# Kernel optimization log

Measured on AMD Instinct MI355X. Metric: run time of the kernel, lower is better.

The kernel has to match this reference:

```python
import jax, jax.numpy as jnp
import numpy as np

B, T = 512, 100
STATE, LATENT, HIDDEN, EMBED, ACT = 200, 30, 200, 1024, 6


def _lin(k, out_dim, in_dim):
    return jax.random.normal(k, (out_dim, in_dim), jnp.float32) / np.sqrt(in_dim)


def setup_inputs() -> dict:
    key = jax.random.key(0)
    ks = jax.random.split(key, 12)
    return {
        "e": jax.random.normal(ks[0], (B, T + 1, EMBED), jnp.float32),
        "u": jax.random.normal(ks[1], (B, T, ACT), jnp.float32),
        "lat_act_W": _lin(ks[2], STATE, LATENT + ACT),
        "lat_act_b": jnp.zeros((STATE,), jnp.float32),
        "gru_Wih": _lin(ks[3], 3 * STATE, STATE),
        "gru_Whh": _lin(ks[4], 3 * STATE, STATE),
        "gru_bih": jnp.zeros((3 * STATE,), jnp.float32),
        "gru_bhh": jnp.zeros((3 * STATE,), jnp.float32),
        "prior1_W": _lin(ks[5], HIDDEN, STATE),
        "prior1_b": jnp.zeros((HIDDEN,), jnp.float32),
        "prior_m_W": _lin(ks[6], LATENT, HIDDEN),
        "prior_m_b": jnp.zeros((LATENT,), jnp.float32),
        "prior_s_W": _lin(ks[7], LATENT, HIDDEN),
        "prior_s_b": jnp.zeros((LATENT,), jnp.float32),
        "post1_W": _lin(ks[8], HIDDEN, STATE + EMBED),
        "post1_b": jnp.zeros((HIDDEN,), jnp.float32),
        "post_m_W": _lin(ks[9], LATENT, HIDDEN),
        "post_m_b": jnp.zeros((LATENT,), jnp.float32),
        "post_s_W": _lin(ks[10], LATENT, HIDDEN),
        "post_s_b": jnp.zeros((LATENT,), jnp.float32),
    }


def _std(raw):
    # softplus(raw) + 0.1, clamped to [1e-6, 10.0]
    return jnp.clip(jax.nn.softplus(raw) + 0.1, 1e-6, 10.0)


def reference(e, u, lat_act_W, lat_act_b, gru_Wih, gru_Whh, gru_bih, gru_bhh,
              prior1_W, prior1_b, prior_m_W, prior_m_b, prior_s_W, prior_s_b,
              post1_W, post1_b, post_m_W, post_m_b, post_s_W, post_s_b):
    Bx = u.shape[0]
    h0 = jnp.zeros((Bx, STATE), u.dtype)
    s0 = jnp.zeros((Bx, LATENT), u.dtype)
    u_t = jnp.swapaxes(u, 0, 1)            # [T, B, A]
    e_t = jnp.swapaxes(e[:, 1:], 0, 1)     # [T, B, E]

    def step(carry, inp):
        h, s = carry
        a, et = inp
        # deterministic_state_fwd
        x = jax.nn.relu(jnp.concatenate([s, a], axis=1) @ lat_act_W.T + lat_act_b)
        gi = x @ gru_Wih.T + gru_bih
        gh = h @ gru_Whh.T + gru_bhh
        ir, iz, inn = jnp.split(gi, 3, axis=1)
        hr, hz, hn = jnp.split(gh, 3, axis=1)
        r = jax.nn.sigmoid(ir + hr)
        z = jax.nn.sigmoid(iz + hz)
        n = jnp.tanh(inn + r * hn)
        h_new = (1.0 - z) * n + z * h
        # prior
        zp = jax.nn.relu(h_new @ prior1_W.T + prior1_b)
        pm = zp @ prior_m_W.T + prior_m_b
        ps = _std(zp @ prior_s_W.T + prior_s_b)
        # posterior
        zq = jax.nn.relu(jnp.concatenate([h_new, et], axis=1) @ post1_W.T + post1_b)
        qm = zq @ post_m_W.T + post_m_b
        qs = _std(zq @ post_s_W.T + post_s_b)
        return (h_new, qm), (h_new, pm, ps, qm, qs)

    _, (states, pm, ps, qm, qs) = jax.lax.scan(step, (h0, s0), (u_t, e_t))
    return states, pm, ps, qm, qs
```

## Files before the change

### kernel.cpp

```cpp
#include <hip/hip_runtime.h>
#include <cstdint>

typedef unsigned int u32;
typedef unsigned short u16;
typedef short bf16x8 __attribute__((ext_vector_type(8)));
typedef float f32x4 __attribute__((ext_vector_type(4)));

#define Bq 512
#define Tq 100
#define NST 200
#define NLAT 30
#define NEMB 1024
#define NACT 6

#define T_LA   0
#define T_IH   26
#define T_HH   299
#define T_P1   572
#define T_PM   663
#define T_POST 677
#define T_PR1  1093
#define T_TOT  1184
#define NFRAG  (T_TOT * 64)

__device__ __forceinline__ u16 f2bf(float f){
  u32 x = __float_as_uint(f);
  return (u16)((x + 0x7FFFu + ((x >> 16) & 1u)) >> 16);
}
__device__ __forceinline__ float bf2f(u16 h){ return __uint_as_float(((u32)h) << 16); }

__device__ __forceinline__ float sigm(float x){ return 1.0f / (1.0f + expf(-x)); }
__device__ __forceinline__ float stdf_(float x){
  float sp = fmaxf(x, 0.f) + log1pf(expf(-fabsf(x))) + 0.1f;
  return fminf(fmaxf(sp, 1e-6f), 10.0f);
}

#define BAR() do { \
  asm volatile("s_waitcnt lgkmcnt(0)" ::: "memory"); \
  __builtin_amdgcn_s_barrier(); \
  asm volatile("" ::: "memory"); \
} while (0)

#define LOAD7(dst, base, unit) do { \
  const u16* _p = (base) + ((((size_t)(unit))*7) << 9) + lane*8; \
  _Pragma("unroll") \
  for (int _k = 0; _k < 7; ++_k) dst[_k] = *(const bf16x8*)(_p + ((size_t)_k << 9)); \
} while (0)

#define CHAIN7(accv, Afr, buf) do { \
  _Pragma("unroll") \
  for (int _k = 0; _k < 7; ++_k) \
    accv = __builtin_amdgcn_mfma_f32_16x16x32_bf16(Afr[_k], buf[_k], accv, 0, 0, 0); \
} while (0)

__global__ __launch_bounds__(256) void prep2(
    const float* __restrict__ lat_act_W,
    const float* __restrict__ gru_Wih,
    const float* __restrict__ gru_Whh,
    const float* __restrict__ post1_W,
    const float* __restrict__ post_m_W,
    const float* __restrict__ prior1_W,
    u16* __restrict__ wbuf)
{
  int gid = blockIdx.x * 256 + threadIdx.x;
  if (gid >= NFRAG) return;
  int tile = gid >> 6, lane = gid & 63;
  int nl = lane & 15, qq = lane >> 4;
  const float* src = nullptr;
  long stride = 0; int row = 0, kbase = 0, kmax = 0, coff = 0; bool vn = false;
  if (tile < T_IH){
    int lt = tile, nt = lt >> 1, kt = lt & 1;
    row = nt*16 + nl; vn = row < 200; kbase = kt*32 + qq*8; kmax = 36;
    src = lat_act_W; stride = 36;
  } else if (tile < T_HH){
    int lt = tile - T_IH, nt = lt / 7, kt = lt - nt*7;
    int g = nt / 3, gate = nt - g*3, nn = g*16 + nl;
    vn = nn < 200; row = gate*200 + nn; kbase = kt*32 + qq*8; kmax = 200;
    src = gru_Wih; stride = 200;
  } else if (tile < T_P1){
    int lt = tile - T_HH, nt = lt / 7, kt = lt - nt*7;
    int g = nt / 3, gate = nt - g*3, nn = g*16 + nl;
    vn = nn < 200; row = gate*200 + nn; kbase = kt*32 + qq*8; kmax = 200;
    src = gru_Whh; stride = 200;
  } else if (tile < T_PM){
    int lt = tile - T_P1, nt = lt / 7, kt = lt - nt*7;
    row = nt*16 + nl; vn = row < 200; kbase = kt*32 + qq*8; kmax = 200;
    src = post1_W; stride = 1224;
  } else if (tile < T_POST){
    int lt = tile - T_PM, nt = lt / 7, kt = lt - nt*7;
    row = nt*16 + nl; vn = row < 30; kbase = kt*32 + qq*8; kmax = 200;
    src = post_m_W; stride = 200;
  } else if (tile < T_PR1){
    int lt = tile - T_POST, nt = lt >> 5, kt = lt & 31;
    row = nt*16 + nl; vn = row < 200; kbase = kt*32 + qq*8; kmax = 1024; coff = 200;
    src = post1_W; stride = 1224;
  } else {
    int lt = tile - T_PR1, nt = lt / 7, kt = lt - nt*7;
    row = nt*16 + nl; vn = row < 200; kbase = kt*32 + qq*8; kmax = 200;
    src = prior1_W; stride = 200;
  }
  __align__(16) u16 ov[8];
  #pragma unroll
  for (int j = 0; j < 8; ++j){
    int k = kbase + j;
    float v = (vn && k < kmax) ? src[(size_t)row*stride + coff + k] : 0.f;
    ov[j] = f2bf(v);
  }
  *(uint4*)(wbuf + (size_t)gid*8) = *(const uint4*)ov;
}

__global__ __launch_bounds__(256) void epost_kernel(
    const float* __restrict__ e,
    const float* __restrict__ post1_b,
    const u16* __restrict__ wbuf,
    u16* __restrict__ Epost)
{
  __shared__ __align__(16) u16 Ab[2][64][40];
  const int tid = threadIdx.x;
  const int wave = tid >> 6, lane = tid & 63, nl = lane & 15, q = lane >> 4;
  const int m0 = blockIdx.x * 64;
  const int tt = m0 >> 9;
  const int b0 = m0 & 511;
  const u16* wPOST = wbuf + (size_t)T_POST * 512;

  f32x4 zero4 = {0.f, 0.f, 0.f, 0.f};
  f32x4 acc[13];
  #pragma unroll
  for (int i = 0; i < 13; ++i) acc[i] = zero4;

  const int sr = tid >> 2;
  const int sc = (tid & 3) * 8;
  const float* esrc = e + ((size_t)(b0 + sr)*(Tq + 1) + (tt + 1))*NEMB + sc;

  {
    float4 f0 = *(const float4*)(esrc);
    float4 f1 = *(const float4*)(esrc + 4);
    bf16x8 v;
    v[0]=(short)f2bf(f0.x); v[1]=(short)f2bf(f0.y); v[2]=(short)f2bf(f0.z); v[3]=(short)f2bf(f0.w);
    v[4]=(short)f2bf(f1.x); v[5]=(short)f2bf(f1.y); v[6]=(short)f2bf(f1.z); v[7]=(short)f2bf(f1.w);
    *(bf16x8*)(&Ab[0][sr][sc]) = v;
  }
  __syncthreads();
  for (int kt = 0; kt < 32; ++kt){
    int cur = kt & 1;
    if (kt + 1 < 32){
      const float* p = esrc + (size_t)(kt + 1)*32;
      float4 f0 = *(const float4*)(p);
      float4 f1 = *(const float4*)(p + 4);
      bf16x8 v;
      v[0]=(short)f2bf(f0.x); v[1]=(short)f2bf(f0.y); v[2]=(short)f2bf(f0.z); v[3]=(short)f2bf(f0.w);
      v[4]=(short)f2bf(f1.x); v[5]=(short)f2bf(f1.y); v[6]=(short)f2bf(f1.z); v[7]=(short)f2bf(f1.w);
      *(bf16x8*)(&Ab[cur ^ 1][sr][sc]) = v;
    }
    bf16x8 afr = *(const bf16x8*)(&Ab[cur][wave*16 + nl][q*8]);
    #pragma unroll
    for (int nt = 0; nt < 13; ++nt){
      bf16x8 b = *(const bf16x8*)(wPOST + (((size_t)(nt*32 + kt)) << 9) + lane*8);
      acc[nt] = __builtin_amdgcn_mfma_f32_16x16x32_bf16(afr, b, acc[nt], 0, 0, 0);
    }
    __syncthreads();
  }
  #pragma unroll
  for (int nt = 0; nt < 13; ++nt){
    int n = nt*16 + nl;
    if (n < 200){
      float bb = post1_b[n];
      #pragma unroll
      for (int r = 0; r < 4; ++r){
        int m = m0 + wave*16 + q*4 + r;
        Epost[(size_t)m*NST + n] = f2bf(acc[nt][r] + bb);
      }
    }
  }
}

__global__ __launch_bounds__(512, 2) void core_kernel(
    const float* __restrict__ u,
    const float* __restrict__ lat_act_b,
    const float* __restrict__ gru_bih,
    const float* __restrict__ gru_bhh,
    const float* __restrict__ post_m_b,
    const u16* __restrict__ wbuf,
    const u16* __restrict__ Epost,
    float* __restrict__ out_states,
    float* __restrict__ out_qm)
{
  __shared__ __align__(16) u16 xs[16][72];
  __shared__ __align__(16) u16 xb[16][232];
  __shared__ __align__(16) u16 hb[2][16][232];
  __shared__ __align__(16) u16 zqb[16][232];

  const int tid  = threadIdx.x;
  const int wave = tid >> 6;
  const int lane = tid & 63;
  const int nl   = lane & 15;
  const int q    = lane >> 4;
  const int row0 = blockIdx.x * 16;

  const u16* wLA = wbuf + (size_t)T_LA * 512;
  const u16* wIH = wbuf + (size_t)T_IH * 512;
  const u16* wHH = wbuf + (size_t)T_HH * 512;
  const u16* wP1 = wbuf + (size_t)T_P1 * 512;
  const u16* wPM = wbuf + (size_t)T_PM * 512;

  for (int i = tid; i < 16*72;  i += 512) ((u16*)xs)[i] = 0;
  for (int i = tid; i < 16*232; i += 512){
    ((u16*)xb)[i] = 0; ((u16*)hb[0])[i] = 0; ((u16*)hb[1])[i] = 0; ((u16*)zqb)[i] = 0;
  }

  const bool two  = (wave < 5);
  const int  cmax = two ? 2 : 1;

  bf16x8 laf[2][2] = {};
  float latb_r[2] = {0.f, 0.f};
  float bih_r[2][3] = {}, bhh_r[2][3] = {};
  #pragma unroll
  for (int c = 0; c < 2; ++c){
    if (c < cmax){
      const int nt = wave + 8*c;
      #pragma unroll
      for (int kt = 0; kt < 2; ++kt)
        laf[c][kt] = *(const bf16x8*)(wLA + (((size_t)(nt*2 + kt)) << 9) + lane*8);
      const int n = nt*16 + nl;
      const bool v = (n < 200);
      latb_r[c] = v ? lat_act_b[n] : 0.f;
      #pragma unroll
      for (int gg = 0; gg < 3; ++gg){
        bih_r[c][gg] = v ? gru_bih[gg*200 + n] : 0.f;
        bhh_r[c][gg] = v ? gru_bhh[gg*200 + n] : 0.f;
      }
    }
  }
  float pmb_r = 0.f;
  { const int n2 = wave*16 + nl; if (wave < 2 && n2 < 30) pmb_r = post_m_b[n2]; }

  float hreg[2][4] = {};

  const int ur = tid / 6, uk = tid - ur*6;
  const bool uth = (tid < 96);
  float u_reg = uth ? u[((size_t)(row0 + ur)*Tq + 0)*NACT + uk] : 0.f;

  bf16x8 bbA[7], bbB[7];
  LOAD7(bbA, wIH, wave*3);

  BAR();

  for (int t = 0; t < Tq; ++t){
    const int pb = t & 1;
    if (uth) xs[ur][30 + uk] = f2bf(u_reg);
    BAR();

    u32 ep0[4], ep1[4];
    {
      const int n0 = wave*16 + nl;
      const int n1 = n0 + 128;
      const u16* eb = Epost + ((size_t)t*Bq + row0 + q*4)*NST;
      #pragma unroll
      for (int r = 0; r < 4; ++r){
        ep0[r] = eb[(size_t)r*NST + n0];
        ep1[r] = (two && n1 < 200) ? (u32)eb[(size_t)r*NST + n1] : 0u;
      }
    }

    {
      bf16x8 a0 = *(const bf16x8*)(&xs[nl][q*8]);
      bf16x8 a1 = *(const bf16x8*)(&xs[nl][32 + q*8]);
      #pragma unroll
      for (int c = 0; c < 2; ++c){
        if (c < cmax){
          f32x4 a = {0.f, 0.f, 0.f, 0.f};
          a = __builtin_amdgcn_mfma_f32_16x16x32_bf16(a0, laf[c][0], a, 0, 0, 0);
          a = __builtin_amdgcn_mfma_f32_16x16x32_bf16(a1, laf[c][1], a, 0, 0, 0);
          const int n = (wave + 8*c)*16 + nl;
          if (n < 200){
            #pragma unroll
            for (int r = 0; r < 4; ++r)
              xb[q*4 + r][n] = f2bf(fmaxf(a[r] + latb_r[c], 0.f));
          }
        }
      }
    }
    BAR();

    {
      bf16x8 ax[7], ah[7];
      #pragma unroll
      for (int kt = 0; kt < 7; ++kt){
        ax[kt] = *(const bf16x8*)(&xb[nl][kt*32 + q*8]);
        ah[kt] = *(const bf16x8*)(&hb[pb][nl][kt*32 + q*8]);
      }
      if (uth && t + 1 < Tq) u_reg = u[((size_t)(row0 + ur)*Tq + (t + 1))*NACT + uk];

      #pragma unroll
      for (int c = 0; c < 2; ++c){
        if (c < cmax){
          const int g  = wave + 8*c;
          const int gu = g*3;
          f32x4 acc0  = {0.f,0.f,0.f,0.f};
          f32x4 acc1  = {0.f,0.f,0.f,0.f};
          f32x4 acc2i = {0.f,0.f,0.f,0.f};
          f32x4 acc2h = {0.f,0.f,0.f,0.f};
          LOAD7(bbB, wHH, gu + 0);
          CHAIN7(acc0, ax, bbA);
          LOAD7(bbA, wIH, gu + 1);
          CHAIN7(acc0, ah, bbB);
          LOAD7(bbB, wHH, gu + 1);
          CHAIN7(acc1, ax, bbA);
          LOAD7(bbA, wIH, gu + 2);
          CHAIN7(acc1, ah, bbB);
          LOAD7(bbB, wHH, gu + 2);
          CHAIN7(acc2i, ax, bbA);
          if (c == 0 && cmax == 2) LOAD7(bbA, wIH, (g + 8)*3);
          else                     LOAD7(bbA, wP1, wave);
          CHAIN7(acc2h, ah, bbB);

          const int n = g*16 + nl;
          if (n < 200){
            #pragma unroll
            for (int r = 0; r < 4; ++r){
              const int m = q*4 + r;
              float rg = sigm(acc0[r] + bih_r[c][0] + bhh_r[c][0]);
              float zg = sigm(acc1[r] + bih_r[c][1] + bhh_r[c][1]);
              float ng = tanhf(acc2i[r] + bih_r[c][2] + rg*(acc2h[r] + bhh_r[c][2]));
              float hn = (1.f - zg)*ng + zg*hreg[c][r];
              hreg[c][r] = hn;
              hb[pb ^ 1][m][n] = f2bf(hn);
              out_states[((size_t)t*Bq + row0 + m)*NST + n] = hn;
            }
          }
        }
      }
    }
    BAR();

    {
      bf16x8 ah2[7];
      #pragma unroll
      for (int kt = 0; kt < 7; ++kt)
        ah2[kt] = *(const bf16x8*)(&hb[pb ^ 1][nl][kt*32 + q*8]);
      f32x4 aP0 = {0.f,0.f,0.f,0.f}, aP1 = {0.f,0.f,0.f,0.f};
      if (two) LOAD7(bbB, wP1, wave + 8);
      CHAIN7(aP0, ah2, bbA);
      if (two){
        if (wave < 2) LOAD7(bbA, wPM, wave);
        else          LOAD7(bbA, wIH, wave*3);
        CHAIN7(aP1, ah2, bbB);
      } else {
        LOAD7(bbA, wIH, wave*3);
      }
      {
        const int n0 = wave*16 + nl;
        #pragma unroll
        for (int r = 0; r < 4; ++r)
          zqb[q*4 + r][n0] = f2bf(fmaxf(aP0[r] + bf2f((u16)ep0[r]), 0.f));
        if (two){
          const int n1 = n0 + 128;
          if (n1 < 200){
            #pragma unroll
            for (int r = 0; r < 4; ++r)
              zqb[q*4 + r][n1] = f2bf(fmaxf(aP1[r] + bf2f((u16)ep1[r]), 0.f));
          }
        }
      }
    }
    BAR();

    if (wave < 2){
      bf16x8 az[7];
      #pragma unroll
      for (int kt = 0; kt < 7; ++kt)
        az[kt] = *(const bf16x8*)(&zqb[nl][kt*32 + q*8]);
      f32x4 aQ = {0.f,0.f,0.f,0.f};
      CHAIN7(aQ, az, bbA);
      const int n = wave*16 + nl;
      if (n < 30){
        #pragma unroll
        for (int r = 0; r < 4; ++r){
          const int m = q*4 + r;
          float v = aQ[r] + pmb_r;
          out_qm[((size_t)t*Bq + row0 + m)*NLAT + n] = v;
          xs[m][n] = f2bf(v);
        }
      }
      LOAD7(bbA, wIH, wave*3);
    }
  }
}

__global__ __launch_bounds__(256) void phasec_kernel(
    const float* __restrict__ states,
    const u16* __restrict__ Epost,
    const u16* __restrict__ wbuf,
    const float* __restrict__ prior1_b,
    const float* __restrict__ prior_m_W, const float* __restrict__ prior_m_b,
    const float* __restrict__ prior_s_W, const float* __restrict__ prior_s_b,
    const float* __restrict__ post_s_W,  const float* __restrict__ post_s_b,
    float* __restrict__ pm, float* __restrict__ ps, float* __restrict__ qs)
{
  __shared__ __align__(16) u16 stb[32][232];
  __shared__ float zp[32][208];
  __shared__ float zqf[32][208];
  const int tid = threadIdx.x, wave = tid >> 6, lane = tid & 63, nl = lane & 15, q = lane >> 4;
  const size_t m0 = (size_t)blockIdx.x * 32;
  const u16* wP1  = wbuf + (size_t)T_P1 * 512;
  const u16* wPR1 = wbuf + (size_t)T_PR1 * 512;

  for (int i = tid; i < 32*200; i += 256){
    int r = i / 200, c = i - r*200;
    stb[r][c] = f2bf(states[(m0 + r)*NST + c]);
  }
  for (int i = tid; i < 32*32; i += 256){
    int r = i >> 5, c = i & 31;
    stb[r][200 + c] = 0;
  }
  __syncthreads();

  {
    const int rowb = (wave & 1) * 16;
    const bool doZQ = (wave >= 2);
    const u16* wmat = doZQ ? wP1 : wPR1;
    bf16x8 a7[7];
    #pragma unroll
    for (int kt = 0; kt < 7; ++kt)
      a7[kt] = *(const bf16x8*)(&stb[rowb + nl][kt*32 + q*8]);
    for (int nt = 0; nt < 13; ++nt){
      f32x4 a = {0.f, 0.f, 0.f, 0.f};
      #pragma unroll
      for (int kt = 0; kt < 7; ++kt){
        bf16x8 b = *(const bf16x8*)(wmat + (((size_t)(nt*7 + kt)) << 9) + lane*8);
        a = __builtin_amdgcn_mfma_f32_16x16x32_bf16(a7[kt], b, a, 0, 0, 0);
      }
      int n = nt*16 + nl;
      if (n < 200){
        #pragma unroll
        for (int r = 0; r < 4; ++r){
          int m = rowb + q*4 + r;
          if (doZQ){
            float v = a[r] + bf2f(Epost[(m0 + m)*NST + n]);
            zqf[m][n] = fmaxf(v, 0.f);
          } else {
            float v = a[r] + prior1_b[n];
            zp[m][n] = fmaxf(v, 0.f);
          }
        }
      }
    }
  }
  __syncthreads();

  for (int i = tid; i < 32*90; i += 256){
    int r = i / 90, rem = i - r*90;
    int head = rem / 30, l = rem - head*30;
    const float* wrow = (head == 0 ? prior_m_W : head == 1 ? prior_s_W : post_s_W) + (size_t)l*NST;
    const float* vec = (head == 2) ? &zqf[r][0] : &zp[r][0];
    float acc = 0.f;
    #pragma unroll 10
    for (int c = 0; c < 50; ++c){
      float4 wv = *(const float4*)(wrow + c*4);
      acc = fmaf(wv.x, vec[c*4 + 0], acc);
      acc = fmaf(wv.y, vec[c*4 + 1], acc);
      acc = fmaf(wv.z, vec[c*4 + 2], acc);
      acc = fmaf(wv.w, vec[c*4 + 3], acc);
    }
    float bias = (head == 0 ? prior_m_b : head == 1 ? prior_s_b : post_s_b)[l];
    float v = acc + bias;
    if (head) v = stdf_(v);
    float* o = head == 0 ? pm : head == 1 ? ps : qs;
    o[(m0 + r)*NLAT + l] = v;
  }
}

extern "C" void kernel_launch(void* const* d_in, const int* in_sizes, int n_in,
                              void* d_out, int out_size, void* d_ws, size_t ws_size,
                              hipStream_t stream)
{
  const float* e         = (const float*)d_in[0];
  const float* u         = (const float*)d_in[1];
  const float* lat_act_W = (const float*)d_in[2];
  const float* lat_act_b = (const float*)d_in[3];
  const float* gru_Wih   = (const float*)d_in[4];
  const float* gru_Whh   = (const float*)d_in[5];
  const float* gru_bih   = (const float*)d_in[6];
  const float* gru_bhh   = (const float*)d_in[7];
  const float* prior1_W  = (const float*)d_in[8];
  const float* prior1_b  = (const float*)d_in[9];
  const float* prior_m_W = (const float*)d_in[10];
  const float* prior_m_b = (const float*)d_in[11];
  const float* prior_s_W = (const float*)d_in[12];
  const float* prior_s_b = (const float*)d_in[13];
  const float* post1_W   = (const float*)d_in[14];
  const float* post1_b   = (const float*)d_in[15];
  const float* post_m_W  = (const float*)d_in[16];
  const float* post_m_b  = (const float*)d_in[17];
  const float* post_s_W  = (const float*)d_in[18];
  const float* post_s_b  = (const float*)d_in[19];

  float* out    = (float*)d_out;
  float* states = out;
  float* pm     = out + 10240000;
  float* ps     = out + 11776000;
  float* qm     = out + 13312000;
  float* qs     = out + 14848000;

  u16* Epost = (u16*)d_ws;
  u16* wbuf  = (u16*)((char*)d_ws + 20480000);

  hipLaunchKernelGGL(prep2, dim3((NFRAG + 255) / 256), dim3(256), 0, stream,
                     lat_act_W, gru_Wih, gru_Whh, post1_W, post_m_W, prior1_W, wbuf);

  hipLaunchKernelGGL(epost_kernel, dim3(800), dim3(256), 0, stream,
                     e, post1_b, wbuf, Epost);

  hipLaunchKernelGGL(core_kernel, dim3(32), dim3(512), 0, stream,
                     u, lat_act_b, gru_bih, gru_bhh, post_m_b, wbuf, Epost, states, qm);

  hipLaunchKernelGGL(phasec_kernel, dim3(1600), dim3(256), 0, stream,
                     states, Epost, wbuf, prior1_b,
                     prior_m_W, prior_m_b, prior_s_W, prior_s_b,
                     post_s_W, post_s_b, pm, ps, qs);
}
```

Before: 1.958 ms.

## Retune GRU core pipeline, fast gate math, direct-load epost, LDS head weights

Several independent changes. The epost GEMM now reads each wave's A fragment straight from global memory and drops the LDS staging and per-step barriers. The core GRU kernel uses three weight buffers to prefetch deeper and hoists the h fragment loads earlier. Gate math switches to v_exp/v_rcp sigmoid and tanh with pre-summed r/z biases. phasec stages the 90x200 head weights in LDS (72KB extra), which may cut its occupancy.

```diff
diff --git a/kernel.cpp b/kernel.cpp
--- a/kernel.cpp
+++ b/kernel.cpp
@@ -29,7 +29,12 @@
 }
 __device__ __forceinline__ float bf2f(u16 h){ return __uint_as_float(((u32)h) << 16); }
 
-__device__ __forceinline__ float sigm(float x){ return 1.0f / (1.0f + expf(-x)); }
+__device__ __forceinline__ float fexp2(float x){ float r; asm("v_exp_f32 %0, %1" : "=v"(r) : "v"(x)); return r; }
+__device__ __forceinline__ float frcp (float x){ float r; asm("v_rcp_f32 %0, %1" : "=v"(r) : "v"(x)); return r; }
+#define LOG2E 1.44269504f
+__device__ __forceinline__ float fsigm(float x){ return frcp(1.0f + fexp2(-LOG2E * x)); }
+__device__ __forceinline__ float ftanh(float x){ return 1.0f - 2.0f * frcp(1.0f + fexp2(2.0f * LOG2E * x)); }
+
 __device__ __forceinline__ float stdf_(float x){
   float sp = fmaxf(x, 0.f) + log1pf(expf(-fabsf(x))) + 0.1f;
   return fminf(fmaxf(sp, 1e-6f), 10.0f);
@@ -115,50 +120,30 @@
     const u16* __restrict__ wbuf,
     u16* __restrict__ Epost)
 {
-  __shared__ __align__(16) u16 Ab[2][64][40];
   const int tid = threadIdx.x;
   const int wave = tid >> 6, lane = tid & 63, nl = lane & 15, q = lane >> 4;
   const int m0 = blockIdx.x * 64;
   const int tt = m0 >> 9;
-  const int b0 = m0 & 511;
-  const u16* wPOST = wbuf + (size_t)T_POST * 512;
-
-  f32x4 zero4 = {0.f, 0.f, 0.f, 0.f};
+  const int b0 = (m0 & 511) + wave*16;
+  const u16* wPOST = wbuf + (size_t)T_POST * 512 + lane*8;
+
   f32x4 acc[13];
   #pragma unroll
-  for (int i = 0; i < 13; ++i) acc[i] = zero4;
-
-  const int sr = tid >> 2;
-  const int sc = (tid & 3) * 8;
-  const float* esrc = e + ((size_t)(b0 + sr)*(Tq + 1) + (tt + 1))*NEMB + sc;
-
-  {
-    float4 f0 = *(const float4*)(esrc);
-    float4 f1 = *(const float4*)(esrc + 4);
-    bf16x8 v;
-    v[0]=(short)f2bf(f0.x); v[1]=(short)f2bf(f0.y); v[2]=(short)f2bf(f0.z); v[3]=(short)f2bf(f0.w);
-    v[4]=(short)f2bf(f1.x); v[5]=(short)f2bf(f1.y); v[6]=(short)f2bf(f1.z); v[7]=(short)f2bf(f1.w);
-    *(bf16x8*)(&Ab[0][sr][sc]) = v;
-  }
-  __syncthreads();
+  for (int i = 0; i < 13; ++i) acc[i] = (f32x4){0.f,0.f,0.f,0.f};
+
+  const float* arow = e + ((size_t)(b0 + nl)*(Tq + 1) + (tt + 1))*NEMB + q*8;
+
   for (int kt = 0; kt < 32; ++kt){
-    int cur = kt & 1;
-    if (kt + 1 < 32){
-      const float* p = esrc + (size_t)(kt + 1)*32;
-      float4 f0 = *(const float4*)(p);
-      float4 f1 = *(const float4*)(p + 4);
-      bf16x8 v;
-      v[0]=(short)f2bf(f0.x); v[1]=(short)f2bf(f0.y); v[2]=(short)f2bf(f0.z); v[3]=(short)f2bf(f0.w);
-      v[4]=(short)f2bf(f1.x); v[5]=(short)f2bf(f1.y); v[6]=(short)f2bf(f1.z); v[7]=(short)f2bf(f1.w);
-      *(bf16x8*)(&Ab[cur ^ 1][sr][sc]) = v;
-    }
-    bf16x8 afr = *(const bf16x8*)(&Ab[cur][wave*16 + nl][q*8]);
+    float4 f0 = *(const float4*)(arow + (size_t)kt*32);
+    float4 f1 = *(const float4*)(arow + (size_t)kt*32 + 4);
+    bf16x8 afr;
+    afr[0]=(short)f2bf(f0.x); afr[1]=(short)f2bf(f0.y); afr[2]=(short)f2bf(f0.z); afr[3]=(short)f2bf(f0.w);
+    afr[4]=(short)f2bf(f1.x); afr[5]=(short)f2bf(f1.y); afr[6]=(short)f2bf(f1.z); afr[7]=(short)f2bf(f1.w);
     #pragma unroll
     for (int nt = 0; nt < 13; ++nt){
-      bf16x8 b = *(const bf16x8*)(wPOST + (((size_t)(nt*32 + kt)) << 9) + lane*8);
+      bf16x8 b = *(const bf16x8*)(wPOST + (((size_t)(nt*32 + kt)) << 9));
       acc[nt] = __builtin_amdgcn_mfma_f32_16x16x32_bf16(afr, b, acc[nt], 0, 0, 0);
     }
-    __syncthreads();
   }
   #pragma unroll
   for (int nt = 0; nt < 13; ++nt){
@@ -203,17 +188,22 @@
   const u16* wP1 = wbuf + (size_t)T_P1 * 512;
   const u16* wPM = wbuf + (size_t)T_PM * 512;
 
+  const bool two  = (wave < 5);
+  const int  cmax = two ? 2 : 1;
+
+  bf16x8 b0[7], b1[7], b2[7];
+  LOAD7(b0, wIH, wave*3);
+  LOAD7(b1, wHH, wave*3);
+
   for (int i = tid; i < 16*72;  i += 512) ((u16*)xs)[i] = 0;
   for (int i = tid; i < 16*232; i += 512){
     ((u16*)xb)[i] = 0; ((u16*)hb[0])[i] = 0; ((u16*)hb[1])[i] = 0; ((u16*)zqb)[i] = 0;
   }
 
-  const bool two  = (wave < 5);
-  const int  cmax = two ? 2 : 1;
-
   bf16x8 laf[2][2] = {};
   float latb_r[2] = {0.f, 0.f};
-  float bih_r[2][3] = {}, bhh_r[2][3] = {};
+  float brz_r[2][2] = {};
+  float bin_r[2] = {}, bhn_r[2] = {};
   #pragma unroll
   for (int c = 0; c < 2; ++c){
     if (c < cmax){
@@ -224,10 +214,11 @@
       const int n = nt*16 + nl;
       const bool v = (n < 200);
       latb_r[c] = v ? lat_act_b[n] : 0.f;
-      #pragma unroll
-      for (int gg = 0; gg < 3; ++gg){
-        bih_r[c][gg] = v ? gru_bih[gg*200 + n] : 0.f;
-        bhh_r[c][gg] = v ? gru_bhh[gg*200 + n] : 0.f;
+      if (v){
+        brz_r[c][0] = gru_bih[n]       + gru_bhh[n];
+        brz_r[c][1] = gru_bih[200 + n] + gru_bhh[200 + n];
+        bin_r[c]    = gru_bih[400 + n];
+        bhn_r[c]    = gru_bhh[400 + n];
       }
     }
   }
@@ -239,9 +230,6 @@
   const int ur = tid / 6, uk = tid - ur*6;
   const bool uth = (tid < 96);
   float u_reg = uth ? u[((size_t)(row0 + ur)*Tq + 0)*NACT + uk] : 0.f;
-
-  bf16x8 bbA[7], bbB[7];
-  LOAD7(bbA, wIH, wave*3);
 
   BAR();
 
@@ -261,6 +249,11 @@
         ep1[r] = (two && n1 < 200) ? (u32)eb[(size_t)r*NST + n1] : 0u;
       }
     }
+
+    bf16x8 ah[7];
+    #pragma unroll
+    for (int kt = 0; kt < 7; ++kt)
+      ah[kt] = *(const bf16x8*)(&hb[pb][nl][kt*32 + q*8]);
 
     {
       bf16x8 a0 = *(const bf16x8*)(&xs[nl][q*8]);
@@ -283,13 +276,13 @@
     BAR();
 
     {
-      bf16x8 ax[7], ah[7];
-      #pragma unroll
-      for (int kt = 0; kt < 7; ++kt){
+      bf16x8 ax[7];
+      #pragma unroll
+      for (int kt = 0; kt < 7; ++kt)
         ax[kt] = *(const bf16x8*)(&xb[nl][kt*32 + q*8]);
-        ah[kt] = *(const bf16x8*)(&hb[pb][nl][kt*32 + q*8]);
-      }
       if (uth && t + 1 < Tq) u_reg = u[((size_t)(row0 + ur)*Tq + (t + 1))*NACT + uk];
+
+      float* os = out_states + ((size_t)t*Bq + row0)*NST;
 
       #pragma unroll
       for (int c = 0; c < 2; ++c){
@@ -300,32 +293,29 @@
           f32x4 acc1  = {0.f,0.f,0.f,0.f};
           f32x4 acc2i = {0.f,0.f,0.f,0.f};
           f32x4 acc2h = {0.f,0.f,0.f,0.f};
-          LOAD7(bbB, wHH, gu + 0);
-          CHAIN7(acc0, ax, bbA);
-          LOAD7(bbA, wIH, gu + 1);
-          CHAIN7(acc0, ah, bbB);
-          LOAD7(bbB, wHH, gu + 1);
-          CHAIN7(acc1, ax, bbA);
-          LOAD7(bbA, wIH, gu + 2);
-          CHAIN7(acc1, ah, bbB);
-          LOAD7(bbB, wHH, gu + 2);
-          CHAIN7(acc2i, ax, bbA);
-          if (c == 0 && cmax == 2) LOAD7(bbA, wIH, (g + 8)*3);
-          else                     LOAD7(bbA, wP1, wave);
-          CHAIN7(acc2h, ah, bbB);
+          LOAD7(b2, wIH, gu + 1);  CHAIN7(acc0, ax, b0);
+          LOAD7(b0, wHH, gu + 1);  CHAIN7(acc0, ah, b1);
+          LOAD7(b1, wIH, gu + 2);  CHAIN7(acc1, ax, b2);
+          LOAD7(b2, wHH, gu + 2);  CHAIN7(acc1, ah, b0);
+          if (c == 0 && two) { LOAD7(b0, wIH, (wave + 8)*3); }
+          else               { LOAD7(b0, wP1, wave); }
+          CHAIN7(acc2i, ax, b1);
+          if (c == 0 && two)      { LOAD7(b1, wHH, (wave + 8)*3); }
+          else if (two)           { LOAD7(b1, wP1, wave + 8); }
+          CHAIN7(acc2h, ah, b2);
 
           const int n = g*16 + nl;
           if (n < 200){
             #pragma unroll
             for (int r = 0; r < 4; ++r){
               const int m = q*4 + r;
-              float rg = sigm(acc0[r] + bih_r[c][0] + bhh_r[c][0]);
-              float zg = sigm(acc1[r] + bih_r[c][1] + bhh_r[c][1]);
-              float ng = tanhf(acc2i[r] + bih_r[c][2] + rg*(acc2h[r] + bhh_r[c][2]));
+              float rg = fsigm(acc0[r] + brz_r[c][0]);
+              float zg = fsigm(acc1[r] + brz_r[c][1]);
+              float ng = ftanh(acc2i[r] + bin_r[c] + rg*(acc2h[r] + bhn_r[c]));
               float hn = (1.f - zg)*ng + zg*hreg[c][r];
               hreg[c][r] = hn;
               hb[pb ^ 1][m][n] = f2bf(hn);
-              out_states[((size_t)t*Bq + row0 + m)*NST + n] = hn;
+              os[(size_t)m*NST + n] = hn;
             }
           }
         }
@@ -339,15 +329,11 @@
       for (int kt = 0; kt < 7; ++kt)
         ah2[kt] = *(const bf16x8*)(&hb[pb ^ 1][nl][kt*32 + q*8]);
       f32x4 aP0 = {0.f,0.f,0.f,0.f}, aP1 = {0.f,0.f,0.f,0.f};
-      if (two) LOAD7(bbB, wP1, wave + 8);
-      CHAIN7(aP0, ah2, bbA);
-      if (two){
-        if (wave < 2) LOAD7(bbA, wPM, wave);
-        else          LOAD7(bbA, wIH, wave*3);
-        CHAIN7(aP1, ah2, bbB);
-      } else {
-        LOAD7(bbA, wIH, wave*3);
-      }
+      if (wave < 2) { LOAD7(b2, wPM, wave); }
+      CHAIN7(aP0, ah2, b0);
+      LOAD7(b0, wIH, wave*3);
+      if (two) { CHAIN7(aP1, ah2, b1); }
+      LOAD7(b1, wHH, wave*3);
       {
         const int n0 = wave*16 + nl;
         #pragma unroll
@@ -371,18 +357,18 @@
       for (int kt = 0; kt < 7; ++kt)
         az[kt] = *(const bf16x8*)(&zqb[nl][kt*32 + q*8]);
       f32x4 aQ = {0.f,0.f,0.f,0.f};
-      CHAIN7(aQ, az, bbA);
+      CHAIN7(aQ, az, b2);
       const int n = wave*16 + nl;
       if (n < 30){
+        float* oq = out_qm + ((size_t)t*Bq + row0)*NLAT;
         #pragma unroll
         for (int r = 0; r < 4; ++r){
           const int m = q*4 + r;
           float v = aQ[r] + pmb_r;
-          out_qm[((size_t)t*Bq + row0 + m)*NLAT + n] = v;
+          oq[(size_t)m*NLAT + n] = v;
           xs[m][n] = f2bf(v);
         }
       }
-      LOAD7(bbA, wIH, wave*3);
     }
   }
 }
@@ -400,6 +386,7 @@
   __shared__ __align__(16) u16 stb[32][232];
   __shared__ float zp[32][208];
   __shared__ float zqf[32][208];
+  __shared__ float hw[90][200];
   const int tid = threadIdx.x, wave = tid >> 6, lane = tid & 63, nl = lane & 15, q = lane >> 4;
   const size_t m0 = (size_t)blockIdx.x * 32;
   const u16* wP1  = wbuf + (size_t)T_P1 * 512;
@@ -412,6 +399,12 @@
   for (int i = tid; i < 32*32; i += 256){
     int r = i >> 5, c = i & 31;
     stb[r][200 + c] = 0;
+  }
+  for (int i = tid; i < 90*200; i += 256){
+    int hl = i / 200, c = i - hl*200;
+    const float* src = (hl < 30) ? prior_m_W : (hl < 60) ? prior_s_W : post_s_W;
+    int l = (hl < 30) ? hl : (hl < 60) ? hl - 30 : hl - 60;
+    ((float*)hw)[i] = src[(size_t)l*NST + c];
   }
   __syncthreads();
 
@@ -451,16 +444,15 @@
   for (int i = tid; i < 32*90; i += 256){
     int r = i / 90, rem = i - r*90;
     int head = rem / 30, l = rem - head*30;
-    const float* wrow = (head == 0 ? prior_m_W : head == 1 ? prior_s_W : post_s_W) + (size_t)l*NST;
+    const float* wrow = &hw[head*30 + l][0];
     const float* vec = (head == 2) ? &zqf[r][0] : &zp[r][0];
     float acc = 0.f;
     #pragma unroll 10
     for (int c = 0; c < 50; ++c){
-      float4 wv = *(const float4*)(wrow + c*4);
-      acc = fmaf(wv.x, vec[c*4 + 0], acc);
-      acc = fmaf(wv.y, vec[c*4 + 1], acc);
-      acc = fmaf(wv.z, vec[c*4 + 2], acc);
-      acc = fmaf(wv.w, vec[c*4 + 3], acc);
+      acc = fmaf(wrow[c*4 + 0], vec[c*4 + 0], acc);
+      acc = fmaf(wrow[c*4 + 1], vec[c*4 + 1], acc);
+      acc = fmaf(wrow[c*4 + 2], vec[c*4 + 2], acc);
+      acc = fmaf(wrow[c*4 + 3], vec[c*4 + 3], acc);
     }
     float bias = (head == 0 ? prior_m_b : head == 1 ? prior_s_b : post_s_b)[l];
     float v = acc + bias;
```

After: 1.949 ms. No clear change (-0.4%).
